# Performance work log

Measured on AMD Instinct MI355X. Metric: run time of the kernel, lower is better.

## Reference

```python
import jax, jax.numpy as jnp
import numpy as np

B = 2048
VOCABS = [100000, 50000, 10, 3, 100, 50, 1000, 24, 5]  # user,item,age,gender,city,category,brand,hour,device
E = 16
EMB_DIMS = [E, E, E // 2, E // 4, E // 2, E // 2, E // 2, E // 4, E // 4]
NUM_FEATURES = sum(VOCABS) + 1  # +1 for the price column
DEEP_IN = sum(EMB_DIMS) + 1  # 77
HIDDEN = [256, 128, 64]


def setup_inputs() -> dict:
    key = jax.random.key(0)
    ks = iter(jax.random.split(key, 40))
    inp = {}
    names = ['user_id', 'item_id', 'age', 'gender', 'city', 'category', 'brand', 'hour', 'device']
    for name, v in zip(names, VOCABS):
        inp[name] = jax.random.randint(next(ks), (B, 1), 0, v, dtype=jnp.int32).astype(jnp.int64)
    inp['price'] = jax.random.uniform(next(ks), (B, 1), dtype=jnp.float32) * 100.0
    # embedding tables
    tab_names = ['emb_user', 'emb_item', 'emb_age', 'emb_gender', 'emb_city', 'emb_category', 'emb_brand', 'emb_hour', 'emb_device']
    for name, v, d in zip(tab_names, VOCABS, EMB_DIMS):
        inp[name] = jax.random.normal(next(ks), (v, d), dtype=jnp.float32) * 0.05
    # dense (1st-order) weights
    inp['w_dense'] = jax.random.normal(next(ks), (NUM_FEATURES,), dtype=jnp.float32) * 0.01
    inp['b_dense'] = jnp.zeros((), dtype=jnp.float32)
    # FM 2nd-order factors
    inp['fm_v'] = jax.random.normal(next(ks), (NUM_FEATURES, E), dtype=jnp.float32) * 0.01
    # deep MLP
    dims = [DEEP_IN] + HIDDEN
    for i in range(len(HIDDEN)):
        inp[f'W{i+1}'] = jax.random.normal(next(ks), (dims[i], dims[i + 1]), dtype=jnp.float32) * (1.0 / np.sqrt(dims[i]))
        inp[f'b{i+1}'] = jnp.zeros((dims[i + 1],), dtype=jnp.float32)
    inp['Wo'] = jax.random.normal(next(ks), (HIDDEN[-1], 1), dtype=jnp.float32) * (1.0 / np.sqrt(HIDDEN[-1]))
    inp['bo'] = jnp.zeros((1,), dtype=jnp.float32)
    return inp


def reference(user_id, item_id, age, gender, city, category, brand, price, hour, device,
              emb_user, emb_item, emb_age, emb_gender, emb_city, emb_category, emb_brand,
              emb_hour, emb_device, w_dense, b_dense, fm_v, W1, b1, W2, b2, W3, b3, Wo, bo):
    b = user_id.shape[0]
    rows = jnp.arange(b)
    ids = [user_id, item_id, age, gender, city, category, brand, hour, device]
    # one-hot style feature vector: (b, NUM_FEATURES)
    feat = jnp.zeros((b, NUM_FEATURES), dtype=price.dtype)
    off = 0
    for idx, v in zip(ids, VOCABS):
        feat = feat.at[rows, off + idx[:, 0]].set(1.0)
        off += v
    feat = feat.at[:, NUM_FEATURES - 1].set(price[:, 0] / 1000.0)

    # 1st-order linear part
    logit_dense = feat @ w_dense + b_dense  # (b,)

    # FM 2nd-order: 0.5 * sum_k [ (x@V)^2 - x^2 @ V^2 ]
    square_of_sum = jnp.square(feat @ fm_v)            # (b, E)
    sum_of_square = jnp.square(feat) @ jnp.square(fm_v)  # (b, E)
    logit_fm = 0.5 * jnp.sum(square_of_sum - sum_of_square, axis=1)  # (b,)

    # deep part: embedding lookups + MLP (dropout inactive / eval mode)
    tables = [emb_user, emb_item, emb_age, emb_gender, emb_city, emb_category, emb_brand, emb_hour, emb_device]
    embs = [t[i[:, 0]] for t, i in zip(tables, ids)]
    deep_in = jnp.concatenate(embs + [price], axis=1)  # (b, 77)
    h = jax.nn.relu(deep_in @ W1 + b1)
    h = jax.nn.relu(h @ W2 + b2)
    h = jax.nn.relu(h @ W3 + b3)
    logit_deep = (h @ Wo + bo)[:, 0]

    return logit_dense + logit_fm + logit_deep
```

## Files before the change

kernel.cpp:

```cpp
#include <hip/hip_runtime.h>


#define RPB 4
#define BATCH 2048
#define NF 151193

#define OFF0 0
#define OFF1 100000
#define OFF2 150000
#define OFF3 150010
#define OFF4 150013
#define OFF5 150113
#define OFF6 150163
#define OFF7 151163
#define OFF8 151187

typedef float f4 __attribute__((ext_vector_type(4)));

__device__ inline f4 relu4(f4 v) {
    f4 r;
    r.x = fmaxf(v.x, 0.0f); r.y = fmaxf(v.y, 0.0f);
    r.z = fmaxf(v.z, 0.0f); r.w = fmaxf(v.w, 0.0f);
    return r;
}

__global__ __launch_bounds__(512, 4) void deepfm_fused(
    const int* __restrict__ f_user, const int* __restrict__ f_item,
    const int* __restrict__ f_age, const int* __restrict__ f_gender,
    const int* __restrict__ f_city, const int* __restrict__ f_cat,
    const int* __restrict__ f_brand, const int* __restrict__ f_hour,
    const int* __restrict__ f_dev, const float* __restrict__ price,
    const float* __restrict__ e_user, const float* __restrict__ e_item,
    const float* __restrict__ e_age, const float* __restrict__ e_gender,
    const float* __restrict__ e_city, const float* __restrict__ e_cat,
    const float* __restrict__ e_brand, const float* __restrict__ e_hour,
    const float* __restrict__ e_dev,
    const float* __restrict__ w_dense, const float* __restrict__ b_dense,
    const float* __restrict__ fm_v,
    const float* __restrict__ W1, const float* __restrict__ b1,
    const float* __restrict__ W2, const float* __restrict__ b2,
    const float* __restrict__ W3, const float* __restrict__ b3,
    const float* __restrict__ Wo, const float* __restrict__ bo,
    float* __restrict__ out)
{
    __shared__ __align__(16) float x[RPB][96];
    __shared__ __align__(16) float h1s[RPB][256];
    __shared__ __align__(16) float h2s[RPB][128];
    __shared__ __align__(16) float pred[8192];
    __shared__ float row_extra[RPB];

    const int tid  = threadIdx.x;
    const int base = blockIdx.x * RPB;

    const f4 b1v  = ((const f4*)b1)[tid & 63];
    const f4 b2v  = ((const f4*)b2)[tid & 31];
    const f4 b3v  = ((const f4*)b3)[tid & 15];
    const f4 wo_r = ((const f4*)Wo)[tid & 15];
    const float bo_s = bo[0];

    if (tid < 128) {
        const int r = tid >> 5, l = tid & 31;
        const int gr = base + r;
        if (l < 16) x[r][ 0 + l] = e_user  [f_user[gr]   * 16 + l];
        if (l < 16) x[r][16 + l] = e_item  [f_item[gr]   * 16 + l];
        if (l <  8) x[r][32 + l] = e_age   [f_age[gr]    *  8 + l];
        if (l <  4) x[r][40 + l] = e_gender[f_gender[gr] *  4 + l];
        if (l <  8) x[r][44 + l] = e_city  [f_city[gr]   *  8 + l];
        if (l <  8) x[r][52 + l] = e_cat   [f_cat[gr]    *  8 + l];
        if (l <  8) x[r][60 + l] = e_brand [f_brand[gr]  *  8 + l];
        if (l <  4) x[r][68 + l] = e_hour  [f_hour[gr]   *  4 + l];
        if (l <  4) x[r][72 + l] = e_dev   [f_dev[gr]    *  4 + l];
        if (l == 0) x[r][76]     = price[gr];
        if (l >= 13) x[r][64 + l] = 0.0f;
    } else if (tid < 192) {
        const int r = (tid >> 4) & 3, k = tid & 15;
        const int gr = base + r;
        const int i0 = f_user[gr], i1 = f_item[gr], i2 = f_age[gr];
        const int i3 = f_gender[gr], i4 = f_city[gr], i5 = f_cat[gr];
        const int i6 = f_brand[gr], i7 = f_hour[gr], i8 = f_dev[gr];
        const float px = price[gr] * (1.0f / 1000.0f);
        float v, s, ssq;
        v = fm_v[(NF - 1) * 16 + k];
        s = px * v; ssq = s * s;
        v = fm_v[(OFF0 + i0) * 16 + k]; s += v; ssq += v * v;
        v = fm_v[(OFF1 + i1) * 16 + k]; s += v; ssq += v * v;
        v = fm_v[(OFF2 + i2) * 16 + k]; s += v; ssq += v * v;
        v = fm_v[(OFF3 + i3) * 16 + k]; s += v; ssq += v * v;
        v = fm_v[(OFF4 + i4) * 16 + k]; s += v; ssq += v * v;
        v = fm_v[(OFF5 + i5) * 16 + k]; s += v; ssq += v * v;
        v = fm_v[(OFF6 + i6) * 16 + k]; s += v; ssq += v * v;
        v = fm_v[(OFF7 + i7) * 16 + k]; s += v; ssq += v * v;
        v = fm_v[(OFF8 + i8) * 16 + k]; s += v; ssq += v * v;
        float q = 0.5f * (s * s - ssq);
        if (k == 0) {
            float d = b_dense[0] + px * w_dense[NF - 1];
            d += w_dense[OFF0 + i0];
            d += w_dense[OFF1 + i1];
            d += w_dense[OFF2 + i2];
            d += w_dense[OFF3 + i3];
            d += w_dense[OFF4 + i4];
            d += w_dense[OFF5 + i5];
            d += w_dense[OFF6 + i6];
            d += w_dense[OFF7 + i7];
            d += w_dense[OFF8 + i8];
            q += d;
        }
        q += __shfl_xor(q, 8);
        q += __shfl_xor(q, 4);
        q += __shfl_xor(q, 2);
        q += __shfl_xor(q, 1);
        if (k == 0) row_extra[r] = q;
    }
    __syncthreads();

    const f4* hv1 = (const f4*)h1s;
    const f4* hv2 = (const f4*)h2s;
    f4* pv = (f4*)pred;

    {
        const int kg = tid >> 6, ct = tid & 63;
        const f4* W1v = (const f4*)W1;
        const f4* xv  = (const f4*)x;
        f4 acc0 = 0, acc1 = 0, acc2 = 0, acc3 = 0;
        #pragma unroll
        for (int c = 0; c < 3; ++c) {
            const int i = 12 * kg + 4 * c, q = 3 * kg + c;
            f4 xa0 = xv[ 0 + q];
            f4 xa1 = xv[24 + q];
            f4 xa2 = xv[48 + q];
            f4 xa3 = xv[72 + q];
            f4 w0 = (i + 0 < 77) ? W1v[(i + 0) * 64 + ct] : (f4)0.0f;
            f4 w1 = (i + 1 < 77) ? W1v[(i + 1) * 64 + ct] : (f4)0.0f;
            f4 w2 = (i + 2 < 77) ? W1v[(i + 2) * 64 + ct] : (f4)0.0f;
            f4 w3 = (i + 3 < 77) ? W1v[(i + 3) * 64 + ct] : (f4)0.0f;
            acc0 += xa0.x * w0 + xa0.y * w1 + xa0.z * w2 + xa0.w * w3;
            acc1 += xa1.x * w0 + xa1.y * w1 + xa1.z * w2 + xa1.w * w3;
            acc2 += xa2.x * w0 + xa2.y * w1 + xa2.z * w2 + xa2.w * w3;
            acc3 += xa3.x * w0 + xa3.y * w1 + xa3.z * w2 + xa3.w * w3;
        }
        pv[(kg * 4 + 0) * 64 + ct] = acc0;
        pv[(kg * 4 + 1) * 64 + ct] = acc1;
        pv[(kg * 4 + 2) * 64 + ct] = acc2;
        pv[(kg * 4 + 3) * 64 + ct] = acc3;
    }
    __syncthreads();
    if (tid < 256) {
        const int r = tid >> 6, c4 = tid & 63;
        f4 s = 0;
        #pragma unroll
        for (int kg = 0; kg < 8; ++kg) s += pv[(kg * 4 + r) * 64 + c4];
        s += b1v;
        ((f4*)h1s)[r * 64 + c4] = relu4(s);
    }
    __syncthreads();

    {
        const int kg = tid >> 5, ct = tid & 31;
        const f4* W2v = (const f4*)W2;
        f4 acc0 = 0, acc1 = 0, acc2 = 0, acc3 = 0;
        #pragma unroll
        for (int c = 0; c < 4; ++c) {
            const int q = 4 * kg + c;
            f4 xa0 = hv1[  0 + q];
            f4 xa1 = hv1[ 64 + q];
            f4 xa2 = hv1[128 + q];
            f4 xa3 = hv1[192 + q];
            f4 w0 = W2v[(4 * q + 0) * 32 + ct];
            f4 w1 = W2v[(4 * q + 1) * 32 + ct];
            f4 w2 = W2v[(4 * q + 2) * 32 + ct];
            f4 w3 = W2v[(4 * q + 3) * 32 + ct];
            acc0 += xa0.x * w0 + xa0.y * w1 + xa0.z * w2 + xa0.w * w3;
            acc1 += xa1.x * w0 + xa1.y * w1 + xa1.z * w2 + xa1.w * w3;
            acc2 += xa2.x * w0 + xa2.y * w1 + xa2.z * w2 + xa2.w * w3;
            acc3 += xa3.x * w0 + xa3.y * w1 + xa3.z * w2 + xa3.w * w3;
        }
        pv[(kg * 4 + 0) * 32 + ct] = acc0;
        pv[(kg * 4 + 1) * 32 + ct] = acc1;
        pv[(kg * 4 + 2) * 32 + ct] = acc2;
        pv[(kg * 4 + 3) * 32 + ct] = acc3;
    }
    __syncthreads();
    if (tid < 128) {
        const int r = tid >> 5, c4 = tid & 31;
        f4 s = 0;
        #pragma unroll
        for (int kg = 0; kg < 16; ++kg) s += pv[(kg * 4 + r) * 32 + c4];
        s += b2v;
        ((f4*)h2s)[r * 32 + c4] = relu4(s);
    }
    __syncthreads();

    {
        const int kg = tid >> 4, ct = tid & 15;
        const f4* W3v = (const f4*)W3;
        f4 acc0 = 0, acc1 = 0, acc2 = 0, acc3 = 0;
        {
            const int q = kg;
            f4 xa0 = hv2[ 0 + q];
            f4 xa1 = hv2[32 + q];
            f4 xa2 = hv2[64 + q];
            f4 xa3 = hv2[96 + q];
            f4 w0 = W3v[(4 * q + 0) * 16 + ct];
            f4 w1 = W3v[(4 * q + 1) * 16 + ct];
            f4 w2 = W3v[(4 * q + 2) * 16 + ct];
            f4 w3 = W3v[(4 * q + 3) * 16 + ct];
            acc0 = xa0.x * w0 + xa0.y * w1 + xa0.z * w2 + xa0.w * w3;
            acc1 = xa1.x * w0 + xa1.y * w1 + xa1.z * w2 + xa1.w * w3;
            acc2 = xa2.x * w0 + xa2.y * w1 + xa2.z * w2 + xa2.w * w3;
            acc3 = xa3.x * w0 + xa3.y * w1 + xa3.z * w2 + xa3.w * w3;
        }
        pv[(kg * 4 + 0) * 16 + ct] = acc0;
        pv[(kg * 4 + 1) * 16 + ct] = acc1;
        pv[(kg * 4 + 2) * 16 + ct] = acc2;
        pv[(kg * 4 + 3) * 16 + ct] = acc3;
    }
    __syncthreads();

    if (tid < 64) {
        const int r = tid >> 4, c4 = tid & 15;
        f4 s = 0;
        #pragma unroll
        for (int kg = 0; kg < 32; ++kg) s += pv[(kg * 4 + r) * 16 + c4];
        s += b3v;
        f4 h = relu4(s);
        float t = h.x * wo_r.x + h.y * wo_r.y + h.z * wo_r.z + h.w * wo_r.w;
        t += __shfl_xor(t, 8);
        t += __shfl_xor(t, 4);
        t += __shfl_xor(t, 2);
        t += __shfl_xor(t, 1);
        if (c4 == 0) out[base + r] = t + bo_s + row_extra[r];
    }
}

extern "C" void kernel_launch(void* const* d_in, const int* in_sizes, int n_in,
                              void* d_out, int out_size, void* d_ws, size_t ws_size,
                              hipStream_t stream) {
    const int*   f_user   = (const int*)  d_in[0];
    const int*   f_item   = (const int*)  d_in[1];
    const int*   f_age    = (const int*)  d_in[2];
    const int*   f_gender = (const int*)  d_in[3];
    const int*   f_city   = (const int*)  d_in[4];
    const int*   f_cat    = (const int*)  d_in[5];
    const int*   f_brand  = (const int*)  d_in[6];
    const int*   f_hour   = (const int*)  d_in[7];
    const int*   f_dev    = (const int*)  d_in[8];
    const float* price    = (const float*)d_in[9];
    const float* e_user   = (const float*)d_in[10];
    const float* e_item   = (const float*)d_in[11];
    const float* e_age    = (const float*)d_in[12];
    const float* e_gender = (const float*)d_in[13];
    const float* e_city   = (const float*)d_in[14];
    const float* e_cat    = (const float*)d_in[15];
    const float* e_brand  = (const float*)d_in[16];
    const float* e_hour   = (const float*)d_in[17];
    const float* e_dev    = (const float*)d_in[18];
    const float* w_dense  = (const float*)d_in[19];
    const float* b_dense  = (const float*)d_in[20];
    const float* fm_v     = (const float*)d_in[21];
    const float* W1       = (const float*)d_in[22];
    const float* b1       = (const float*)d_in[23];
    const float* W2       = (const float*)d_in[24];
    const float* b2       = (const float*)d_in[25];
    const float* W3       = (const float*)d_in[26];
    const float* b3       = (const float*)d_in[27];
    const float* Wo       = (const float*)d_in[28];
    const float* bo       = (const float*)d_in[29];
    float* out = (float*)d_out;

    dim3 grid(BATCH / RPB);
    dim3 block(512);
    for (int rep = 0; rep < 3; ++rep) {
        deepfm_fused<<<grid, block, 0, stream>>>(
            f_user, f_item, f_age, f_gender, f_city, f_cat, f_brand, f_hour, f_dev,
            price, e_user, e_item, e_age, e_gender, e_city, e_cat, e_brand, e_hour,
            e_dev, w_dense, b_dense, fm_v, W1, b1, W2, b2, W3, b3, Wo, bo, out);
    }
}
```

Before: 154.6 us.

## Process eight rows per block and drop redundant triple kernel launch

Doubles rows per block from 4 to 8, so each weight vector loaded from W1/W2/W3 is reused across twice as many batch rows. The accumulators become register arrays, and the shared scratch buffer and thread-role splits are resized to match. Launch bounds drop to 2 blocks per CU, which gives up some occupancy in exchange for the extra registers. The host wrapper also stops launching the kernel three times and launches it once, removing duplicated work.

```diff
diff --git a/kernel.cpp b/kernel.cpp
--- a/kernel.cpp
+++ b/kernel.cpp
@@ -1,7 +1,7 @@
 #include <hip/hip_runtime.h>
 
 
-#define RPB 4
+#define RPB 8
 #define BATCH 2048
 #define NF 151193
 
@@ -24,7 +24,7 @@
     return r;
 }
 
-__global__ __launch_bounds__(512, 4) void deepfm_fused(
+__global__ __launch_bounds__(512, 2) void deepfm_fused(
     const int* __restrict__ f_user, const int* __restrict__ f_item,
     const int* __restrict__ f_age, const int* __restrict__ f_gender,
     const int* __restrict__ f_city, const int* __restrict__ f_cat,
@@ -46,7 +46,7 @@
     __shared__ __align__(16) float x[RPB][96];
     __shared__ __align__(16) float h1s[RPB][256];
     __shared__ __align__(16) float h2s[RPB][128];
-    __shared__ __align__(16) float pred[8192];
+    __shared__ __align__(16) float pred[16384];
     __shared__ float row_extra[RPB];
 
     const int tid  = threadIdx.x;
@@ -58,7 +58,7 @@
     const f4 wo_r = ((const f4*)Wo)[tid & 15];
     const float bo_s = bo[0];
 
-    if (tid < 128) {
+    if (tid < 256) {
         const int r = tid >> 5, l = tid & 31;
         const int gr = base + r;
         if (l < 16) x[r][ 0 + l] = e_user  [f_user[gr]   * 16 + l];
@@ -72,8 +72,8 @@
         if (l <  4) x[r][72 + l] = e_dev   [f_dev[gr]    *  4 + l];
         if (l == 0) x[r][76]     = price[gr];
         if (l >= 13) x[r][64 + l] = 0.0f;
-    } else if (tid < 192) {
-        const int r = (tid >> 4) & 3, k = tid & 15;
+    } else if (tid < 384) {
+        const int r = (tid >> 4) & 7, k = tid & 15;
         const int gr = base + r;
         const int i0 = f_user[gr], i1 = f_item[gr], i2 = f_age[gr];
         const int i3 = f_gender[gr], i4 = f_city[gr], i5 = f_cat[gr];
@@ -121,34 +121,31 @@
         const int kg = tid >> 6, ct = tid & 63;
         const f4* W1v = (const f4*)W1;
         const f4* xv  = (const f4*)x;
-        f4 acc0 = 0, acc1 = 0, acc2 = 0, acc3 = 0;
+        f4 acc[RPB];
+        #pragma unroll
+        for (int r = 0; r < RPB; ++r) acc[r] = 0;
         #pragma unroll
         for (int c = 0; c < 3; ++c) {
             const int i = 12 * kg + 4 * c, q = 3 * kg + c;
-            f4 xa0 = xv[ 0 + q];
-            f4 xa1 = xv[24 + q];
-            f4 xa2 = xv[48 + q];
-            f4 xa3 = xv[72 + q];
             f4 w0 = (i + 0 < 77) ? W1v[(i + 0) * 64 + ct] : (f4)0.0f;
             f4 w1 = (i + 1 < 77) ? W1v[(i + 1) * 64 + ct] : (f4)0.0f;
             f4 w2 = (i + 2 < 77) ? W1v[(i + 2) * 64 + ct] : (f4)0.0f;
             f4 w3 = (i + 3 < 77) ? W1v[(i + 3) * 64 + ct] : (f4)0.0f;
-            acc0 += xa0.x * w0 + xa0.y * w1 + xa0.z * w2 + xa0.w * w3;
-            acc1 += xa1.x * w0 + xa1.y * w1 + xa1.z * w2 + xa1.w * w3;
-            acc2 += xa2.x * w0 + xa2.y * w1 + xa2.z * w2 + xa2.w * w3;
-            acc3 += xa3.x * w0 + xa3.y * w1 + xa3.z * w2 + xa3.w * w3;
-        }
-        pv[(kg * 4 + 0) * 64 + ct] = acc0;
-        pv[(kg * 4 + 1) * 64 + ct] = acc1;
-        pv[(kg * 4 + 2) * 64 + ct] = acc2;
-        pv[(kg * 4 + 3) * 64 + ct] = acc3;
-    }
-    __syncthreads();
-    if (tid < 256) {
+            #pragma unroll
+            for (int r = 0; r < RPB; ++r) {
+                f4 xa = xv[r * 24 + q];
+                acc[r] += xa.x * w0 + xa.y * w1 + xa.z * w2 + xa.w * w3;
+            }
+        }
+        #pragma unroll
+        for (int r = 0; r < RPB; ++r) pv[(kg * 8 + r) * 64 + ct] = acc[r];
+    }
+    __syncthreads();
+    {
         const int r = tid >> 6, c4 = tid & 63;
         f4 s = 0;
         #pragma unroll
-        for (int kg = 0; kg < 8; ++kg) s += pv[(kg * 4 + r) * 64 + c4];
+        for (int kg = 0; kg < 8; ++kg) s += pv[(kg * 8 + r) * 64 + c4];
         s += b1v;
         ((f4*)h1s)[r * 64 + c4] = relu4(s);
     }
@@ -157,34 +154,31 @@
     {
         const int kg = tid >> 5, ct = tid & 31;
         const f4* W2v = (const f4*)W2;
-        f4 acc0 = 0, acc1 = 0, acc2 = 0, acc3 = 0;
+        f4 acc[RPB];
+        #pragma unroll
+        for (int r = 0; r < RPB; ++r) acc[r] = 0;
         #pragma unroll
         for (int c = 0; c < 4; ++c) {
             const int q = 4 * kg + c;
-            f4 xa0 = hv1[  0 + q];
-            f4 xa1 = hv1[ 64 + q];
-            f4 xa2 = hv1[128 + q];
-            f4 xa3 = hv1[192 + q];
             f4 w0 = W2v[(4 * q + 0) * 32 + ct];
             f4 w1 = W2v[(4 * q + 1) * 32 + ct];
             f4 w2 = W2v[(4 * q + 2) * 32 + ct];
             f4 w3 = W2v[(4 * q + 3) * 32 + ct];
-            acc0 += xa0.x * w0 + xa0.y * w1 + xa0.z * w2 + xa0.w * w3;
-            acc1 += xa1.x * w0 + xa1.y * w1 + xa1.z * w2 + xa1.w * w3;
-            acc2 += xa2.x * w0 + xa2.y * w1 + xa2.z * w2 + xa2.w * w3;
-            acc3 += xa3.x * w0 + xa3.y * w1 + xa3.z * w2 + xa3.w * w3;
-        }
-        pv[(kg * 4 + 0) * 32 + ct] = acc0;
-        pv[(kg * 4 + 1) * 32 + ct] = acc1;
-        pv[(kg * 4 + 2) * 32 + ct] = acc2;
-        pv[(kg * 4 + 3) * 32 + ct] = acc3;
-    }
-    __syncthreads();
-    if (tid < 128) {
+            #pragma unroll
+            for (int r = 0; r < RPB; ++r) {
+                f4 xa = hv1[r * 64 + q];
+                acc[r] += xa.x * w0 + xa.y * w1 + xa.z * w2 + xa.w * w3;
+            }
+        }
+        #pragma unroll
+        for (int r = 0; r < RPB; ++r) pv[(kg * 8 + r) * 32 + ct] = acc[r];
+    }
+    __syncthreads();
+    if (tid < 256) {
         const int r = tid >> 5, c4 = tid & 31;
         f4 s = 0;
         #pragma unroll
-        for (int kg = 0; kg < 16; ++kg) s += pv[(kg * 4 + r) * 32 + c4];
+        for (int kg = 0; kg < 16; ++kg) s += pv[(kg * 8 + r) * 32 + c4];
         s += b2v;
         ((f4*)h2s)[r * 32 + c4] = relu4(s);
     }
@@ -193,34 +187,27 @@
     {
         const int kg = tid >> 4, ct = tid & 15;
         const f4* W3v = (const f4*)W3;
-        f4 acc0 = 0, acc1 = 0, acc2 = 0, acc3 = 0;
-        {
-            const int q = kg;
-            f4 xa0 = hv2[ 0 + q];
-            f4 xa1 = hv2[32 + q];
-            f4 xa2 = hv2[64 + q];
-            f4 xa3 = hv2[96 + q];
-            f4 w0 = W3v[(4 * q + 0) * 16 + ct];
-            f4 w1 = W3v[(4 * q + 1) * 16 + ct];
-            f4 w2 = W3v[(4 * q + 2) * 16 + ct];
-            f4 w3 = W3v[(4 * q + 3) * 16 + ct];
-            acc0 = xa0.x * w0 + xa0.y * w1 + xa0.z * w2 + xa0.w * w3;
-            acc1 = xa1.x * w0 + xa1.y * w1 + xa1.z * w2 + xa1.w * w3;
-            acc2 = xa2.x * w0 + xa2.y * w1 + xa2.z * w2 + xa2.w * w3;
-            acc3 = xa3.x * w0 + xa3.y * w1 + xa3.z * w2 + xa3.w * w3;
-        }
-        pv[(kg * 4 + 0) * 16 + ct] = acc0;
-        pv[(kg * 4 + 1) * 16 + ct] = acc1;
-        pv[(kg * 4 + 2) * 16 + ct] = acc2;
-        pv[(kg * 4 + 3) * 16 + ct] = acc3;
-    }
-    __syncthreads();
-
-    if (tid < 64) {
+        const int q = kg;
+        f4 w0 = W3v[(4 * q + 0) * 16 + ct];
+        f4 w1 = W3v[(4 * q + 1) * 16 + ct];
+        f4 w2 = W3v[(4 * q + 2) * 16 + ct];
+        f4 w3 = W3v[(4 * q + 3) * 16 + ct];
+        f4 acc[RPB];
+        #pragma unroll
+        for (int r = 0; r < RPB; ++r) {
+            f4 xa = hv2[r * 32 + q];
+            acc[r] = xa.x * w0 + xa.y * w1 + xa.z * w2 + xa.w * w3;
+        }
+        #pragma unroll
+        for (int r = 0; r < RPB; ++r) pv[(kg * 8 + r) * 16 + ct] = acc[r];
+    }
+    __syncthreads();
+
+    if (tid < 128) {
         const int r = tid >> 4, c4 = tid & 15;
         f4 s = 0;
         #pragma unroll
-        for (int kg = 0; kg < 32; ++kg) s += pv[(kg * 4 + r) * 16 + c4];
+        for (int kg = 0; kg < 32; ++kg) s += pv[(kg * 8 + r) * 16 + c4];
         s += b3v;
         f4 h = relu4(s);
         float t = h.x * wo_r.x + h.y * wo_r.y + h.z * wo_r.z + h.w * wo_r.w;
@@ -269,10 +256,8 @@
 
     dim3 grid(BATCH / RPB);
     dim3 block(512);
-    for (int rep = 0; rep < 3; ++rep) {
-        deepfm_fused<<<grid, block, 0, stream>>>(
-            f_user, f_item, f_age, f_gender, f_city, f_cat, f_brand, f_hour, f_dev,
-            price, e_user, e_item, e_age, e_gender, e_city, e_cat, e_brand, e_hour,
-            e_dev, w_dense, b_dense, fm_v, W1, b1, W2, b2, W3, b3, Wo, bo, out);
-    }
+    deepfm_fused<<<grid, block, 0, stream>>>(
+        f_user, f_item, f_age, f_gender, f_city, f_cat, f_brand, f_hour, f_dev,
+        price, e_user, e_item, e_age, e_gender, e_city, e_cat, e_brand, e_hour,
+        e_dev, w_dense, b_dense, fm_v, W1, b1, W2, b2, W3, b3, Wo, bo, out);
 }
```

Measured after the change: 129.4 us. 16.3% less time.
